# Optimization experiments

Measured on AMD Instinct MI355X. Metric: run time of the kernel, lower is better.

Reference implementation:

```python
import jax, jax.numpy as jnp
import numpy as np
from jax.scipy.special import logsumexp

SCALE = 10.0
EPS = 1e-05
MARGIN_INTRA = 40.0
MARGIN_INTER = 6.0
K_INTRA = 4   # sorted1[4:]
K_INTER = 6   # sorted2[6:]


def setup_inputs() -> dict:
    key = jax.random.key(0)
    k1, k2 = jax.random.split(key)
    n, d, n_cams = 4096, 256, 8
    feature = jax.random.normal(k1, (n, d), dtype=jnp.float32)
    camid = jax.random.randint(k2, (n,), 0, n_cams, dtype=jnp.int64)
    return {"feature": feature, "camid": camid}


def reference(feature, camid):
    n = feature.shape[0]
    # pairwise Euclidean distances: ||fi||^2 + ||fj||^2 - 2 fi.fj + eps, clamped, sqrt
    sq = jnp.sum(feature * feature, axis=1)                      # [n]
    dist = sq[:, None] + sq[None, :] + EPS - 2.0 * (feature @ feature.T)
    dist = jnp.sqrt(jnp.clip(dist, 1e-12))                       # [n, n]

    same_cam = camid[:, None] == camid[None, :]                  # [n, n] bool
    inf = jnp.array(jnp.inf, dtype=dist.dtype)

    # masked sorts: +inf padding sorts to the end and contributes exp(-inf)=0
    sorted_intra = jnp.sort(jnp.where(same_cam, dist, inf), axis=1)   # [n, n]
    sorted_inter = jnp.sort(jnp.where(same_cam, inf, dist), axis=1)   # [n, n]

    # x = log(sum(exp(-scale * sorted[:1]))) == -scale * sorted[0]
    x_intra = -SCALE * sorted_intra[:, 0]
    y_intra = logsumexp(-SCALE * sorted_intra[:, K_INTRA:], axis=1)
    x_inter = -SCALE * sorted_inter[:, 0]
    y_inter = logsumexp(-SCALE * sorted_inter[:, K_INTER:], axis=1)

    loss_intra = jnp.sum(jnp.maximum(-x_intra + y_intra + MARGIN_INTRA, 0.0))
    loss_inter = jnp.sum(jnp.maximum(-x_inter + y_inter + MARGIN_INTER, 0.0))
    return (loss_intra + 0.5 * loss_inter) / n
```

## Files before the change

### kernel.cpp

```cpp
#include <hip/hip_runtime.h>
#include <hip/hip_bf16.h>
#include <math.h>

#define N 4096
#define D 256
#define SCALEF 10.0f
#define EPSF 1e-5f
#define MARGIN_INTRA 40.0f
#define MARGIN_INTER 6.0f
#define LI 3
#define LX 6
#define NCHUNK 16
#define NSTRIP 64
#define PPARTS (NCHUNK * 2)

#define LOG2EF 1.44269504f
#define LN2F 0.69314718f

typedef unsigned short ushort_t;
typedef __attribute__((ext_vector_type(8))) short short8;
typedef __attribute__((ext_vector_type(4))) float floatx4;

__device__ __forceinline__ ushort_t f2bf(float x) {
    __hip_bfloat16 h = __float2bfloat16(x);
    return *reinterpret_cast<ushort_t*>(&h);
}
__device__ __forceinline__ float bf2f(ushort_t u) {
    __hip_bfloat16 h = *reinterpret_cast<__hip_bfloat16*>(&u);
    return __bfloat162float(h);
}

__device__ __forceinline__ float fast_exp2(float x) {
#if __has_builtin(__builtin_amdgcn_exp2f)
    return __builtin_amdgcn_exp2f(x);
#else
    return exp2f(x);
#endif
}

template <int L>
__device__ __forceinline__ void insert_desc(float (&t)[L], float v) {
    float top = fmaxf(t[0], v);
#pragma unroll
    for (int q = L - 1; q >= 1; --q)
        t[q] = __builtin_amdgcn_fmed3f(t[q - 1], t[q], v);
    t[0] = top;
}

__global__ __launch_bounds__(64) void prep_kernel(const float* __restrict__ F,
                                                  ushort_t* __restrict__ Fhi,
                                                  ushort_t* __restrict__ Flo,
                                                  float* __restrict__ sq,
                                                  float* __restrict__ Rrow,
                                                  float* __restrict__ out) {
    int row = blockIdx.x;
    int lane = threadIdx.x;
    if (row == 0 && lane == 0) out[0] = 0.0f;
    float4 v = ((const float4*)(F + (size_t)row * D))[lane];
    ushort4 h, l;
    h.x = f2bf(v.x); l.x = f2bf(v.x - bf2f(h.x));
    h.y = f2bf(v.y); l.y = f2bf(v.y - bf2f(h.y));
    h.z = f2bf(v.z); l.z = f2bf(v.z - bf2f(h.z));
    h.w = f2bf(v.w); l.w = f2bf(v.w - bf2f(h.w));
    ((ushort4*)(Fhi + (size_t)row * D))[lane] = h;
    ((ushort4*)(Flo + (size_t)row * D))[lane] = l;
    float s = v.x * v.x + v.y * v.y + v.z * v.z + v.w * v.w;
#pragma unroll
    for (int off = 32; off > 0; off >>= 1) s += __shfl_down(s, off, 64);
    if (lane == 0) {
        sq[row] = s;
        Rrow[row] = -SCALEF * sqrtf(2.0f * s);
    }
}

#define LDST 40

template <bool HD>
__device__ __forceinline__ void epi_tile(
    const floatx4 (&acc)[4][2], int j0, int wr, int quad,
    const float (&si)[2], const float (&nR2)[2], const int (&ci4)[2], const int (&ig)[2],
    const float* __restrict__ sq, const int* __restrict__ camid,
    float (&tI)[2][LI], float (&tX)[2][LX], float (&sIa)[2], float (&sXa)[2]) {
    const float C1 = -SCALEF * LOG2EF;
#pragma unroll
    for (int mi = 0; mi < 4; ++mi) {
        int jg0 = j0 + wr * 64 + mi * 16 + quad * 4;
        float4 sj4 = *(const float4*)(sq + jg0);
        int4 cj4 = *(const int4*)(camid + jg0);
        const float* sjp = (const float*)&sj4;
        const int* cjp = (const int*)&cj4;
#pragma unroll
        for (int ni = 0; ni < 2; ++ni) {
            int dd = jg0 - ig[ni];
            float sie = si[ni] + EPSF;
#pragma unroll
            for (int r = 0; r < 4; ++r) {
                float d2 = sie + sjp[r] - 2.0f * acc[mi][ni][r];
                float d = sqrtf(fmaxf(d2, 1e-12f));
                float k = fmaf(d, C1, nR2[ni]);
                float e = fast_exp2(k);
                bool ii = (cjp[r] == ci4[ni]);
                bool okI = HD ? (ii && ((dd + r) != 0)) : ii;
                sIa[ni] += okI ? e : 0.0f;
                sXa[ni] += ii ? 0.0f : e;
                insert_desc<LI>(tI[ni], okI ? k : -INFINITY);
                insert_desc<LX>(tX[ni], ii ? -INFINITY : k);
            }
        }
    }
}

__global__ __launch_bounds__(256, 4) void fused_kernel(
    const ushort_t* __restrict__ Fhi, const ushort_t* __restrict__ Flo,
    const float* __restrict__ sq, const float* __restrict__ Rrow,
    const int* __restrict__ camid,
    float4* __restrict__ partA, float4* __restrict__ partB, float4* __restrict__ partC) {
    __shared__ ushort_t lds[(128 + 128 + 64 + 64) * LDST];
    ushort_t* ldsAh = lds;
    ushort_t* ldsAl = lds + 128 * LDST;
    ushort_t* ldsBh = lds + 256 * LDST;
    ushort_t* ldsBl = lds + 320 * LDST;

    int tid = threadIdx.x;
    int wave = tid >> 6, lane = tid & 63;
    int wr = wave >> 1, wc = wave & 1;
    int lane15 = lane & 15, quad = lane >> 4;
    int cid = blockIdx.x, sid = blockIdx.y;
    int i0 = sid * 64, j00 = cid * 256;

    float si[2], nR2[2];
    int ci4[2], ig[2];
#pragma unroll
    for (int ni = 0; ni < 2; ++ni) {
        int i = i0 + wc * 32 + ni * 16 + lane15;
        ig[ni] = i;
        si[ni] = sq[i];
        nR2[ni] = -Rrow[i] * LOG2EF;
        ci4[ni] = camid[i];
    }

    float tI[2][LI], tX[2][LX], sIa[2], sXa[2];
#pragma unroll
    for (int ni = 0; ni < 2; ++ni) {
#pragma unroll
        for (int q = 0; q < LI; ++q) tI[ni][q] = -INFINITY;
#pragma unroll
        for (int q = 0; q < LX; ++q) tX[ni][q] = -INFINITY;
        sIa[ni] = 0.0f; sXa[ni] = 0.0f;
    }

    int srowA = tid >> 1, shalf = tid & 1;
    int srowB = tid >> 2, squart = tid & 3;
    const ushort_t* gBh = Fhi + (size_t)(i0 + srowB) * D + squart * 8;
    const ushort_t* gBl = Flo + (size_t)(i0 + srowB) * D + squart * 8;
    ushort_t* sdstAh = ldsAh + srowA * LDST + shalf * 16;
    ushort_t* sdstAl = ldsAl + srowA * LDST + shalf * 16;
    ushort_t* sdstBh = ldsBh + srowB * LDST + squart * 8;
    ushort_t* sdstBl = ldsBl + srowB * LDST + squart * 8;

#pragma unroll 1
    for (int jt = 0; jt < 2; ++jt) {
        int j0 = j00 + jt * 128;
        const ushort_t* gAh = Fhi + (size_t)(j0 + srowA) * D + shalf * 16;
        const ushort_t* gAl = Flo + (size_t)(j0 + srowA) * D + shalf * 16;
        floatx4 acc[4][2] = {};

#pragma unroll 1
        for (int kt = 0; kt < 8; ++kt) {
            int koff = kt * 32;
            short8 ra[2], rb[2], rc, rd;
#pragma unroll
            for (int q = 0; q < 2; ++q) {
                ra[q] = *(const short8*)(gAh + koff + q * 8);
                rb[q] = *(const short8*)(gAl + koff + q * 8);
            }
            rc = *(const short8*)(gBh + koff);
            rd = *(const short8*)(gBl + koff);
            __syncthreads();
#pragma unroll
            for (int q = 0; q < 2; ++q) {
                *(short8*)(sdstAh + q * 8) = ra[q];
                *(short8*)(sdstAl + q * 8) = rb[q];
            }
            *(short8*)(sdstBh) = rc;
            *(short8*)(sdstBl) = rd;
            __syncthreads();

            int eoff = quad * 8;
            short8 ahi[4], alo[4];
#pragma unroll
            for (int mi = 0; mi < 4; ++mi) {
                int r = wr * 64 + mi * 16 + lane15;
                ahi[mi] = *(const short8*)(ldsAh + r * LDST + eoff);
                alo[mi] = *(const short8*)(ldsAl + r * LDST + eoff);
            }
#pragma unroll
            for (int ni = 0; ni < 2; ++ni) {
                int r = wc * 32 + ni * 16 + lane15;
                short8 bhi = *(const short8*)(ldsBh + r * LDST + eoff);
                short8 blo = *(const short8*)(ldsBl + r * LDST + eoff);
#pragma unroll
                for (int mi = 0; mi < 4; ++mi) {
                    acc[mi][ni] = __builtin_amdgcn_mfma_f32_16x16x32_bf16(ahi[mi], bhi, acc[mi][ni], 0, 0, 0);
                    acc[mi][ni] = __builtin_amdgcn_mfma_f32_16x16x32_bf16(ahi[mi], blo, acc[mi][ni], 0, 0, 0);
                    acc[mi][ni] = __builtin_amdgcn_mfma_f32_16x16x32_bf16(alo[mi], bhi, acc[mi][ni], 0, 0, 0);
                }
            }
        }

        if (cid == (sid >> 2) && jt == ((sid >> 1) & 1))
            epi_tile<true>(acc, j0, wr, quad, si, nR2, ci4, ig, sq, camid, tI, tX, sIa, sXa);
        else
            epi_tile<false>(acc, j0, wr, quad, si, nR2, ci4, ig, sq, camid, tI, tX, sIa, sXa);
    }

#pragma unroll
    for (int off = 16; off <= 32; off <<= 1) {
#pragma unroll
        for (int ni = 0; ni < 2; ++ni) {
            sIa[ni] += __shfl_xor(sIa[ni], off, 64);
            sXa[ni] += __shfl_xor(sXa[ni], off, 64);
            float oI[LI], oX[LX];
#pragma unroll
            for (int q = 0; q < LI; ++q) oI[q] = __shfl_xor(tI[ni][q], off, 64);
#pragma unroll
            for (int q = 0; q < LX; ++q) oX[q] = __shfl_xor(tX[ni][q], off, 64);
#pragma unroll
            for (int q = 0; q < LI; ++q) insert_desc<LI>(tI[ni], oI[q]);
#pragma unroll
            for (int q = 0; q < LX; ++q) insert_desc<LX>(tX[ni], oX[q]);
        }
    }

    if (quad == 0) {
        int p = cid * 2 + wr;
#pragma unroll
        for (int ni = 0; ni < 2; ++ni) {
            size_t idx = (size_t)p * N + ig[ni];
            partA[idx] = make_float4(tI[ni][0], tI[ni][1], tI[ni][2], sIa[ni]);
            partB[idx] = make_float4(tX[ni][0], tX[ni][1], tX[ni][2], tX[ni][3]);
            partC[idx] = make_float4(tX[ni][4], tX[ni][5], sXa[ni], 0.0f);
        }
    }
}

__global__ __launch_bounds__(256) void merge_kernel(const float4* __restrict__ partA,
                                                    const float4* __restrict__ partB,
                                                    const float4* __restrict__ partC,
                                                    const float* __restrict__ Rrow,
                                                    float* __restrict__ out) {
    int tid = threadIdx.x;
    int row = blockIdx.x * 256 + tid;
    float mI[LI] = {-INFINITY, -INFINITY, -INFINITY};
    float mX[LX] = {-INFINITY, -INFINITY, -INFINITY, -INFINITY, -INFINITY, -INFINITY};
    float SI = 0.0f, SX = 0.0f;
#pragma unroll 4
    for (int p = 0; p < PPARTS; ++p) {
        size_t idx = (size_t)p * N + row;
        float4 a = partA[idx];
        float4 b = partB[idx];
        float4 c = partC[idx];
        insert_desc<LI>(mI, a.x); insert_desc<LI>(mI, a.y); insert_desc<LI>(mI, a.z);
        SI += a.w;
        insert_desc<LX>(mX, b.x); insert_desc<LX>(mX, b.y);
        insert_desc<LX>(mX, b.z); insert_desc<LX>(mX, b.w);
        insert_desc<LX>(mX, c.x); insert_desc<LX>(mX, c.y);
        SX += c.z;
    }
    float R = Rrow[row];
    float subI = fast_exp2(mI[0]) + fast_exp2(mI[1]) + fast_exp2(mI[2]);
    float restI = fmaxf(SI - subI, 1e-37f);
    float yI = R + logf(restI);
    float hI = fmaxf(yI + SCALEF * sqrtf(EPSF) + MARGIN_INTRA, 0.0f);
    float subX = fast_exp2(mX[0]) + fast_exp2(mX[1]) + fast_exp2(mX[2]) +
                 fast_exp2(mX[3]) + fast_exp2(mX[4]) + fast_exp2(mX[5]);
    float restX = fmaxf(SX - subX, 1e-37f);
    float hX = fmaxf(logf(restX) - mX[0] * LN2F + MARGIN_INTER, 0.0f);
    float l = hI + 0.5f * hX;

    __shared__ float sbuf[256];
    sbuf[tid] = l;
    __syncthreads();
    for (int stride = 128; stride > 0; stride >>= 1) {
        if (tid < stride) sbuf[tid] += sbuf[tid + stride];
        __syncthreads();
    }
    if (tid == 0) atomicAdd(out, sbuf[0] * (1.0f / (float)N));
}

extern "C" void kernel_launch(void* const* d_in, const int* in_sizes, int n_in,
                              void* d_out, int out_size, void* d_ws, size_t ws_size,
                              hipStream_t stream) {
    const float* F = (const float*)d_in[0];
    const int* camid = (const int*)d_in[1];
    float* out = (float*)d_out;
    char* ws = (char*)d_ws;

    ushort_t* Fhi = (ushort_t*)ws;
    ushort_t* Flo = Fhi + (size_t)N * D;
    float* sq = (float*)(ws + 2 * (size_t)N * D * 2);
    float* Rrow = sq + N;
    float* rowloss = Rrow + N;
    (void)rowloss;
    float4* partA = (float4*)(ws + 2 * (size_t)N * D * 2 + 3 * N * 4);
    float4* partB = partA + (size_t)PPARTS * N;
    float4* partC = partB + (size_t)PPARTS * N;

    prep_kernel<<<N, 64, 0, stream>>>(F, Fhi, Flo, sq, Rrow, out);
    fused_kernel<<<dim3(NCHUNK, NSTRIP), 256, 0, stream>>>(Fhi, Flo, sq, Rrow, camid,
                                                           partA, partB, partC);
    merge_kernel<<<N / 256, 256, 0, stream>>>(partA, partB, partC, Rrow, out);
}
```

Baseline: 127.6 us.

## Load GEMM tiles with direct global-to-LDS DMA and XOR-swizzled layout

Replaces the register-staged global loads and LDS stores for the hi/lo bf16 A and B tiles with global_load_lds 16-byte direct transfers. The padded LDS layout becomes a dense layout with an XOR swizzle on the column chunk, so the MFMA operand reads avoid bank conflicts. The goal is to cut VGPR pressure and the separate store instructions in the main loop. The kernel is still single-buffered with two barriers per k-step, and it now depends on the swizzle matching between the DMA writes and the LDS reads.

Measured after the change: 125.0 us. 2.1% less time.

```diff
diff --git a/kernel.cpp b/kernel.cpp
--- a/kernel.cpp
+++ b/kernel.cpp
@@ -36,6 +36,12 @@
 #else
     return exp2f(x);
 #endif
+}
+
+__device__ __forceinline__ void dma16(const void* g, void* l) {
+    __builtin_amdgcn_global_load_lds(
+        (const __attribute__((address_space(1))) unsigned int*)g,
+        (__attribute__((address_space(3))) unsigned int*)l, 16, 0, 0);
 }
 
 template <int L>
@@ -73,7 +79,11 @@
     }
 }
 
-#define LDST 40
+#define KCH 32
+#define AH_OFF 0
+#define AL_OFF 4096
+#define BH_OFF 8192
+#define BL_OFF 10240
 
 template <bool HD>
 __device__ __forceinline__ void epi_tile(
@@ -115,11 +125,7 @@
     const float* __restrict__ sq, const float* __restrict__ Rrow,
     const int* __restrict__ camid,
     float4* __restrict__ partA, float4* __restrict__ partB, float4* __restrict__ partC) {
-    __shared__ ushort_t lds[(128 + 128 + 64 + 64) * LDST];
-    ushort_t* ldsAh = lds;
-    ushort_t* ldsAl = lds + 128 * LDST;
-    ushort_t* ldsBh = lds + 256 * LDST;
-    ushort_t* ldsBl = lds + 320 * LDST;
+    __shared__ ushort_t lds[(128 + 128 + 64 + 64) * KCH];
 
     int tid = threadIdx.x;
     int wave = tid >> 6, lane = tid & 63;
@@ -149,56 +155,60 @@
         sIa[ni] = 0.0f; sXa[ni] = 0.0f;
     }
 
-    int srowA = tid >> 1, shalf = tid & 1;
-    int srowB = tid >> 2, squart = tid & 3;
-    const ushort_t* gBh = Fhi + (size_t)(i0 + srowB) * D + squart * 8;
-    const ushort_t* gBl = Flo + (size_t)(i0 + srowB) * D + squart * 8;
-    ushort_t* sdstAh = ldsAh + srowA * LDST + shalf * 16;
-    ushort_t* sdstAl = ldsAl + srowA * LDST + shalf * 16;
-    ushort_t* sdstBh = ldsBh + srowB * LDST + squart * 8;
-    ushort_t* sdstBl = ldsBl + srowB * LDST + squart * 8;
+    const ushort_t* gsrc[6];
+    ushort_t* lb[6];
+    {
+        int rlo = lane >> 2;
+        int qsw = (lane & 3) ^ ((lane >> 3) & 3);
+#pragma unroll
+        for (int it = 0; it < 6; ++it) {
+            int c = wave + 4 * it;
+            lb[it] = (ushort_t*)lds + (size_t)c * 512;
+            const ushort_t* base;
+            int rowg;
+            if (c < 16) {
+                base = (c < 8) ? Fhi : Flo;
+                rowg = j00 + (c & 7) * 16 + rlo;
+            } else {
+                base = (c < 20) ? Fhi : Flo;
+                rowg = i0 + (c & 3) * 16 + rlo;
+            }
+            gsrc[it] = base + (size_t)rowg * D + qsw * 8;
+        }
+    }
+
+    int eswz = (quad ^ ((lane15 >> 1) & 3)) * 8;
 
 #pragma unroll 1
     for (int jt = 0; jt < 2; ++jt) {
         int j0 = j00 + jt * 128;
-        const ushort_t* gAh = Fhi + (size_t)(j0 + srowA) * D + shalf * 16;
-        const ushort_t* gAl = Flo + (size_t)(j0 + srowA) * D + shalf * 16;
+        size_t jadv = (size_t)jt * 128 * D;
         floatx4 acc[4][2] = {};
 
 #pragma unroll 1
         for (int kt = 0; kt < 8; ++kt) {
-            int koff = kt * 32;
-            short8 ra[2], rb[2], rc, rd;
-#pragma unroll
-            for (int q = 0; q < 2; ++q) {
-                ra[q] = *(const short8*)(gAh + koff + q * 8);
-                rb[q] = *(const short8*)(gAl + koff + q * 8);
-            }
-            rc = *(const short8*)(gBh + koff);
-            rd = *(const short8*)(gBl + koff);
+            int koff = kt * KCH;
             __syncthreads();
 #pragma unroll
-            for (int q = 0; q < 2; ++q) {
-                *(short8*)(sdstAh + q * 8) = ra[q];
-                *(short8*)(sdstAl + q * 8) = rb[q];
-            }
-            *(short8*)(sdstBh) = rc;
-            *(short8*)(sdstBl) = rd;
+            for (int it = 0; it < 4; ++it)
+                dma16(gsrc[it] + jadv + koff, lb[it]);
+#pragma unroll
+            for (int it = 4; it < 6; ++it)
+                dma16(gsrc[it] + koff, lb[it]);
             __syncthreads();
 
-            int eoff = quad * 8;
             short8 ahi[4], alo[4];
 #pragma unroll
             for (int mi = 0; mi < 4; ++mi) {
                 int r = wr * 64 + mi * 16 + lane15;
-                ahi[mi] = *(const short8*)(ldsAh + r * LDST + eoff);
-                alo[mi] = *(const short8*)(ldsAl + r * LDST + eoff);
+                ahi[mi] = *(const short8*)((ushort_t*)lds + AH_OFF + r * KCH + eswz);
+                alo[mi] = *(const short8*)((ushort_t*)lds + AL_OFF + r * KCH + eswz);
             }
 #pragma unroll
             for (int ni = 0; ni < 2; ++ni) {
                 int r = wc * 32 + ni * 16 + lane15;
-                short8 bhi = *(const short8*)(ldsBh + r * LDST + eoff);
-                short8 blo = *(const short8*)(ldsBl + r * LDST + eoff);
+                short8 bhi = *(const short8*)((ushort_t*)lds + BH_OFF + r * KCH + eswz);
+                short8 blo = *(const short8*)((ushort_t*)lds + BL_OFF + r * KCH + eswz);
 #pragma unroll
                 for (int mi = 0; mi < 4; ++mi) {
                     acc[mi][ni] = __builtin_amdgcn_mfma_f32_16x16x32_bf16(ahi[mi], bhi, acc[mi][ni], 0, 0, 0);
```

## Sort rows by camera so most epilogue tiles skip intra-camera bookkeeping

Applied to the files above, without the earlier changes.

Adds a single-block counting sort that permutes rows by camera id, gathers features in that sorted order in the prep kernel, and passes per-camera index ranges to the fused kernel. Epilogue 16-column subtiles whose columns fall entirely outside the row strip's camera range take a fast path that only updates the inter-camera sum and top-k, with no camid load, compare or intra bookkeeping. This trims per-element ALU work in the epilogue, at the cost of an extra tiny serial kernel launch and a gather through the permutation. The diagonal/self-exclusion check still relies on sorted indices, which remains consistent because both i and j use the permuted order.

After: 133.3 us. 1.04x slower.

```diff
diff --git a/kernel.cpp b/kernel.cpp
--- a/kernel.cpp
+++ b/kernel.cpp
@@ -4,6 +4,7 @@
 
 #define N 4096
 #define D 256
+#define NCAM 8
 #define SCALEF 10.0f
 #define EPSF 1e-5f
 #define MARGIN_INTRA 40.0f
@@ -47,7 +48,43 @@
     t[0] = top;
 }
 
+__global__ __launch_bounds__(256) void sort_kernel(const int* __restrict__ camid,
+                                                   int* __restrict__ perm,
+                                                   int* __restrict__ sortedCam,
+                                                   int* __restrict__ camLoC,
+                                                   int* __restrict__ camHiC) {
+    __shared__ int hist[NCAM], base[NCAM], cursor[NCAM];
+    int tid = threadIdx.x;
+    if (tid < NCAM) hist[tid] = 0;
+    __syncthreads();
+    int ids[16];
+#pragma unroll
+    for (int q = 0; q < 16; ++q) {
+        ids[q] = camid[tid * 16 + q];
+        atomicAdd(&hist[ids[q]], 1);
+    }
+    __syncthreads();
+    if (tid == 0) {
+        int acc = 0;
+        for (int c = 0; c < NCAM; ++c) {
+            base[c] = acc; cursor[c] = acc;
+            camLoC[c] = acc;
+            acc += hist[c];
+            camHiC[c] = acc;
+        }
+    }
+    __syncthreads();
+#pragma unroll
+    for (int q = 0; q < 16; ++q) {
+        int o = tid * 16 + q;
+        int pos = atomicAdd(&cursor[ids[q]], 1);
+        perm[pos] = o;
+        sortedCam[pos] = ids[q];
+    }
+}
+
 __global__ __launch_bounds__(64) void prep_kernel(const float* __restrict__ F,
+                                                  const int* __restrict__ perm,
                                                   ushort_t* __restrict__ Fhi,
                                                   ushort_t* __restrict__ Flo,
                                                   float* __restrict__ sq,
@@ -56,7 +93,8 @@
     int row = blockIdx.x;
     int lane = threadIdx.x;
     if (row == 0 && lane == 0) out[0] = 0.0f;
-    float4 v = ((const float4*)(F + (size_t)row * D))[lane];
+    int o = perm[row];
+    float4 v = ((const float4*)(F + (size_t)o * D))[lane];
     ushort4 h, l;
     h.x = f2bf(v.x); l.x = f2bf(v.x - bf2f(h.x));
     h.y = f2bf(v.y); l.y = f2bf(v.y - bf2f(h.y));
@@ -77,34 +115,51 @@
 
 template <bool HD>
 __device__ __forceinline__ void epi_tile(
-    const floatx4 (&acc)[4][2], int j0, int wr, int quad,
+    const floatx4 (&acc)[4][2], int j0, int wr, int quad, int uLo, int uHi,
     const float (&si)[2], const float (&nR2)[2], const int (&ci4)[2], const int (&ig)[2],
-    const float* __restrict__ sq, const int* __restrict__ camid,
+    const float* __restrict__ sq, const int* __restrict__ scam,
     float (&tI)[2][LI], float (&tX)[2][LX], float (&sIa)[2], float (&sXa)[2]) {
     const float C1 = -SCALEF * LOG2EF;
 #pragma unroll
     for (int mi = 0; mi < 4; ++mi) {
-        int jg0 = j0 + wr * 64 + mi * 16 + quad * 4;
+        int jb = j0 + wr * 64 + mi * 16;
+        int jg0 = jb + quad * 4;
         float4 sj4 = *(const float4*)(sq + jg0);
-        int4 cj4 = *(const int4*)(camid + jg0);
         const float* sjp = (const float*)&sj4;
-        const int* cjp = (const int*)&cj4;
-#pragma unroll
-        for (int ni = 0; ni < 2; ++ni) {
-            int dd = jg0 - ig[ni];
-            float sie = si[ni] + EPSF;
-#pragma unroll
-            for (int r = 0; r < 4; ++r) {
-                float d2 = sie + sjp[r] - 2.0f * acc[mi][ni][r];
-                float d = sqrtf(fmaxf(d2, 1e-12f));
-                float k = fmaf(d, C1, nR2[ni]);
-                float e = fast_exp2(k);
-                bool ii = (cjp[r] == ci4[ni]);
-                bool okI = HD ? (ii && ((dd + r) != 0)) : ii;
-                sIa[ni] += okI ? e : 0.0f;
-                sXa[ni] += ii ? 0.0f : e;
-                insert_desc<LI>(tI[ni], okI ? k : -INFINITY);
-                insert_desc<LX>(tX[ni], ii ? -INFINITY : k);
+        bool fastTile = (uHi <= jb) || (uLo >= jb + 16);
+        if (fastTile) {
+#pragma unroll
+            for (int ni = 0; ni < 2; ++ni) {
+                float sie = si[ni] + EPSF;
+#pragma unroll
+                for (int r = 0; r < 4; ++r) {
+                    float d2 = sie + sjp[r] - 2.0f * acc[mi][ni][r];
+                    float d = sqrtf(fmaxf(d2, 1e-12f));
+                    float k = fmaf(d, C1, nR2[ni]);
+                    sXa[ni] += fast_exp2(k);
+                    insert_desc<LX>(tX[ni], k);
+                }
+            }
+        } else {
+            int4 cj4 = *(const int4*)(scam + jg0);
+            const int* cjp = (const int*)&cj4;
+#pragma unroll
+            for (int ni = 0; ni < 2; ++ni) {
+                int dd = jg0 - ig[ni];
+                float sie = si[ni] + EPSF;
+#pragma unroll
+                for (int r = 0; r < 4; ++r) {
+                    float d2 = sie + sjp[r] - 2.0f * acc[mi][ni][r];
+                    float d = sqrtf(fmaxf(d2, 1e-12f));
+                    float k = fmaf(d, C1, nR2[ni]);
+                    float e = fast_exp2(k);
+                    bool ii = (cjp[r] == ci4[ni]);
+                    bool okI = HD ? (ii && ((dd + r) != 0)) : ii;
+                    sIa[ni] += okI ? e : 0.0f;
+                    sXa[ni] += ii ? 0.0f : e;
+                    insert_desc<LI>(tI[ni], okI ? k : -INFINITY);
+                    insert_desc<LX>(tX[ni], ii ? -INFINITY : k);
+                }
             }
         }
     }
@@ -113,7 +168,8 @@
 __global__ __launch_bounds__(256, 4) void fused_kernel(
     const ushort_t* __restrict__ Fhi, const ushort_t* __restrict__ Flo,
     const float* __restrict__ sq, const float* __restrict__ Rrow,
-    const int* __restrict__ camid,
+    const int* __restrict__ scam, const int* __restrict__ camLoC,
+    const int* __restrict__ camHiC,
     float4* __restrict__ partA, float4* __restrict__ partB, float4* __restrict__ partC) {
     __shared__ ushort_t lds[(128 + 128 + 64 + 64) * LDST];
     ushort_t* ldsAh = lds;
@@ -136,8 +192,11 @@
         ig[ni] = i;
         si[ni] = sq[i];
         nR2[ni] = -Rrow[i] * LOG2EF;
-        ci4[ni] = camid[i];
-    }
+        ci4[ni] = scam[i];
+    }
+    int rA = i0 + wc * 32;
+    int uLo = camLoC[scam[rA]];
+    int uHi = camHiC[scam[rA + 31]];
 
     float tI[2][LI], tX[2][LX], sIa[2], sXa[2];
 #pragma unroll
@@ -209,9 +268,9 @@
         }
 
         if (cid == (sid >> 2) && jt == ((sid >> 1) & 1))
-            epi_tile<true>(acc, j0, wr, quad, si, nR2, ci4, ig, sq, camid, tI, tX, sIa, sXa);
+            epi_tile<true>(acc, j0, wr, quad, uLo, uHi, si, nR2, ci4, ig, sq, scam, tI, tX, sIa, sXa);
         else
-            epi_tile<false>(acc, j0, wr, quad, si, nR2, ci4, ig, sq, camid, tI, tX, sIa, sXa);
+            epi_tile<false>(acc, j0, wr, quad, uLo, uHi, si, nR2, ci4, ig, sq, scam, tI, tX, sIa, sXa);
     }
 
 #pragma unroll
@@ -305,9 +364,15 @@
     float4* partA = (float4*)(ws + 2 * (size_t)N * D * 2 + 3 * N * 4);
     float4* partB = partA + (size_t)PPARTS * N;
     float4* partC = partB + (size_t)PPARTS * N;
-
-    prep_kernel<<<N, 64, 0, stream>>>(F, Fhi, Flo, sq, Rrow, out);
-    fused_kernel<<<dim3(NCHUNK, NSTRIP), 256, 0, stream>>>(Fhi, Flo, sq, Rrow, camid,
+    int* perm = (int*)(partC + (size_t)PPARTS * N);
+    int* sortedCam = perm + N;
+    int* camLoC = sortedCam + N;
+    int* camHiC = camLoC + NCAM;
+
+    sort_kernel<<<1, 256, 0, stream>>>(camid, perm, sortedCam, camLoC, camHiC);
+    prep_kernel<<<N, 64, 0, stream>>>(F, perm, Fhi, Flo, sq, Rrow, out);
+    fused_kernel<<<dim3(NCHUNK, NSTRIP), 256, 0, stream>>>(Fhi, Flo, sq, Rrow, sortedCam,
+                                                           camLoC, camHiC,
                                                            partA, partB, partC);
     merge_kernel<<<N / 256, 256, 0, stream>>>(partA, partB, partC, Rrow, out);
 }
```
